# Performance work log

Measured on AMD Instinct MI355X. Metric: run time of the kernel, lower is better.

## Reference

```python
import jax, jax.numpy as jnp
import numpy as np

B, T, V, S = 64, 512, 1296, 32
BLANK = 0
NEG = jnp.float32(-1e30)  # log-space -inf surrogate (keeps grads finite)


def setup_inputs() -> dict:
    key = jax.random.key(0)
    k1, k2 = jax.random.split(key)
    logits = jax.random.normal(k1, (B, T, V), dtype=jnp.float32)
    # CTC targets must not contain the blank index (0)
    targets = jax.random.randint(k2, (B, S), 1, V).astype(jnp.int64)
    input_lengths = jnp.full((B,), T, dtype=jnp.int32)
    target_lengths = jnp.full((B,), S, dtype=jnp.int32)
    return {"logits": logits, "targets": targets,
            "input_lengths": input_lengths, "target_lengths": target_lengths}


def _ctc_loss(log_probs, targets, input_lengths, target_lengths):
    """CTC negative log-likelihood, reduction='mean' (per-sample / target_len, then batch mean)."""
    Bb, Tt, Vv = log_probs.shape
    Ss = targets.shape[1]
    L = 2 * Ss + 1  # extended label sequence: blank-interleaved

    ext = jnp.full((Bb, L), BLANK, dtype=targets.dtype).at[:, 1::2].set(targets)  # (B,L)
    # log-prob of each extended label at each time: (B,T,L)
    lp_ext = jnp.take_along_axis(log_probs, jnp.broadcast_to(ext[:, None, :], (Bb, Tt, L)), axis=2)

    # transition s-2 -> s allowed iff ext[s] is non-blank (s odd) and ext[s] != ext[s-2]
    pos = jnp.arange(L)
    ext_m2 = jnp.pad(ext, ((0, 0), (2, 0)), constant_values=-1)[:, :L]
    skip_ok = (pos[None, :] % 2 == 1) & (ext != ext_m2)  # (B,L)

    alpha0 = (jnp.full((Bb, L), NEG)
              .at[:, 0].set(lp_ext[:, 0, 0])
              .at[:, 1].set(lp_ext[:, 0, 1]))

    def step(alpha, lp_t):
        a1 = alpha
        a2 = jnp.pad(alpha[:, :-1], ((0, 0), (1, 0)), constant_values=NEG)
        a3 = jnp.where(skip_ok, jnp.pad(alpha[:, :-2], ((0, 0), (2, 0)), constant_values=NEG), NEG)
        new = jnp.logaddexp(jnp.logaddexp(a1, a2), a3) + lp_t
        return new, new

    _, alphas_rest = jax.lax.scan(step, alpha0, jnp.swapaxes(lp_ext, 0, 1)[1:])  # (T-1,B,L)
    alphas = jnp.concatenate([alpha0[None], alphas_rest], axis=0)  # (T,B,L)

    bi = jnp.arange(Bb)
    alpha_last = alphas[input_lengths - 1, bi]  # (B,L)
    l_end = alpha_last[bi, 2 * target_lengths]       # final blank
    l_lab = alpha_last[bi, 2 * target_lengths - 1]   # final label
    nll = -jnp.logaddexp(l_end, l_lab)               # (B,)
    nll = jnp.where(jnp.isinf(nll) | (nll > 1e29), 0.0, nll)  # zero_infinity=True
    return jnp.mean(nll / target_lengths.astype(nll.dtype))    # reduction='mean'


def reference(logits, targets, input_lengths, target_lengths):
    log_probs = jax.nn.log_softmax(logits, axis=-1)
    return _ctc_loss(log_probs, targets, input_lengths, target_lengths)
```

## Files before the change

kernel.cpp:

```cpp
#include <hip/hip_runtime.h>
#include <math.h>

#define BB 64
#define TT 512
#define VV 1296
#define SS 32
#define NST 64
#define NG  (TT/4)
#define NEGV (-1e30f)
#define LOG2E 1.44269504088896340736f
#define LN2   0.69314718055994530942f

#define EXP2(x) __builtin_amdgcn_exp2f(x)
#define LOG2(x) __builtin_amdgcn_logf(x)

__device__ __forceinline__ float dpp_shr1(float old, float src) {
    return __int_as_float(__builtin_amdgcn_update_dpp(
        __float_as_int(old), __float_as_int(src), 0x138, 0xf, 0xf, false));
}
__device__ __forceinline__ float dpp_shl1(float old, float src) {
    return __int_as_float(__builtin_amdgcn_update_dpp(
        __float_as_int(old), __float_as_int(src), 0x130, 0xf, 0xf, false));
}

template<int CTRL>
__device__ __forceinline__ float dpp_add(float s) {
    return s + __int_as_float(__builtin_amdgcn_update_dpp(
        0, __float_as_int(s), CTRL, 0xf, 0xf, false));
}
__device__ __forceinline__ float wave_sum63(float s) {
    s = dpp_add<0x111>(s);
    s = dpp_add<0x112>(s);
    s = dpp_add<0x114>(s);
    s = dpp_add<0x118>(s);
    s = dpp_add<0x142>(s);
    s = dpp_add<0x143>(s);
    return s;
}

__device__ __forceinline__ float expsum_row(
    float4 a0, float4 a1, float4 a2, float4 a3, float4 a4, float4 ax, int lane)
{
    if (lane >= 4) { ax.x = NEGV; ax.y = NEGV; ax.z = NEGV; ax.w = NEGV; }
    const float t0 = (__expf(a0.x) + __expf(a0.y)) + (__expf(a0.z) + __expf(a0.w));
    const float t1 = (__expf(a1.x) + __expf(a1.y)) + (__expf(a1.z) + __expf(a1.w));
    const float t2 = (__expf(a2.x) + __expf(a2.y)) + (__expf(a2.z) + __expf(a2.w));
    const float t3 = (__expf(a3.x) + __expf(a3.y)) + (__expf(a3.z) + __expf(a3.w));
    const float t4 = (__expf(a4.x) + __expf(a4.y)) + (__expf(a4.z) + __expf(a4.w));
    const float t5 = (__expf(ax.x) + __expf(ax.y)) + (__expf(ax.z) + __expf(ax.w));
    return ((t0 + t1) + (t2 + t3)) + (t4 + t5);
}

__device__ __forceinline__ float finish_row(float s, float g) {
    const float tot = __shfl(wave_sum63(s), 63, 64);
    return __builtin_fmaf(g, LOG2E, -LOG2(tot));
}

__global__ __launch_bounds__(256, 4) void k_lse_gather(
    const float* __restrict__ logits,
    const int* __restrict__ targets,
    float* __restrict__ lp_ext,
    float* __restrict__ out)
{
    const int wid  = threadIdx.x >> 6;
    const int lane = threadIdx.x & 63;
    const int W    = blockIdx.x * 4 + wid;
    const int b    = W >> 7;
    const int g    = W & (NG - 1);

    if (W == 0 && lane == 0) out[0] = 0.f;

    const int lab = (lane & 1) ? 0 : targets[b * SS + (lane >> 1)];

    const float* rowbase = logits + (size_t)(b * TT + g * 4) * VV;
    const float4* r0 = (const float4*)(rowbase);
    const float4* r1 = (const float4*)(rowbase + VV);
    const float4* r2 = (const float4*)(rowbase + 2 * VV);
    const float4* r3 = (const float4*)(rowbase + 3 * VV);

    float4 A0 = r0[lane], A1 = r0[lane + 64], A2 = r0[lane + 128],
           A3 = r0[lane + 192], A4 = r0[lane + 256], Ax = r0[320 + (lane & 3)];
    float  Ag = ((const float*)r0)[lab];
    float4 B0 = r1[lane], B1 = r1[lane + 64], B2 = r1[lane + 128],
           B3 = r1[lane + 192], B4 = r1[lane + 256], Bx = r1[320 + (lane & 3)];
    float  Bg = ((const float*)r1)[lab];
    float4 C0 = r2[lane], C1 = r2[lane + 64], C2 = r2[lane + 128],
           C3 = r2[lane + 192], C4 = r2[lane + 256], Cx = r2[320 + (lane & 3)];
    float  Cg = ((const float*)r2)[lab];
    float4 D0 = r3[lane], D1 = r3[lane + 64], D2 = r3[lane + 128],
           D3 = r3[lane + 192], D4 = r3[lane + 256], Dx = r3[320 + (lane & 3)];
    float  Dg = ((const float*)r3)[lab];

    __builtin_amdgcn_sched_barrier(0);

    const float sA = expsum_row(A0, A1, A2, A3, A4, Ax, lane);
    const float lp0 = finish_row(sA, Ag);
    const float sB = expsum_row(B0, B1, B2, B3, B4, Bx, lane);
    const float lp1 = finish_row(sB, Bg);
    const float sC = expsum_row(C0, C1, C2, C3, C4, Cx, lane);
    const float lp2 = finish_row(sC, Cg);
    const float sD = expsum_row(D0, D1, D2, D3, D4, Dx, lane);
    const float lp3 = finish_row(sD, Dg);

    float4 st; st.x = lp0; st.y = lp1; st.z = lp2; st.w = lp3;
    ((float4*)lp_ext)[(size_t)W * NST + lane] = st;
}

#define PFV 6

__global__ __launch_bounds__(64) void k_alpha(
    const float* __restrict__ lp_ext,
    const int* __restrict__ targets,
    const int* __restrict__ in_len,
    const int* __restrict__ tgt_len,
    float* __restrict__ out)
{
    const int b    = blockIdx.x;
    const int lane = threadIdx.x;
    const float4* lpv = (const float4*)(lp_ext + (size_t)b * NG * NST * 4);
    const int Ti = in_len[b];
    const int Sb = tgt_len[b];

    bool skip = false;
    if (!(lane & 1) && lane >= 2) {
        const int j = lane >> 1;
        skip = (targets[b * SS + j] != targets[b * SS + j - 1]);
    }

    const float4 g0 = lpv[lane];

    float alpha = (lane == 0) ? g0.x : NEGV;
    float c0    = __shfl(g0.x, 1, 64);

#define STEP(LPS)                                                            \
    {                                                                        \
        const float lps_ = (LPS);                                            \
           \
        const float lpbk_ = (lane & 1) ? lps_ : dpp_shl1(lps_, lps_);        \
        const float a1_ = alpha;                                             \
        const float a2_ = dpp_shr1(c0, alpha);         \
        float a3_       = dpp_shr1(NEGV, a2_);               \
        a3_ = skip ? a3_ : NEGV;          \
        c0 += lpbk_;                                     \
        const float mx_ = fmaxf(fmaxf(a1_, a2_), a3_);           \
        const float ml_ = mx_ + lps_;                 \
        alpha = LOG2(EXP2(a1_ - mx_) + EXP2(a2_ - mx_) +                     \
                     EXP2(a3_ - mx_)) + ml_;                                 \
    }

    if (Ti > 1) STEP(g0.y);
    if (Ti > 2) STEP(g0.z);
    if (Ti > 3) STEP(g0.w);

    float4 bufv[PFV];
    #pragma unroll
    for (int i = 0; i < PFV; ++i) {
        int gg = 1 + i; if (gg > NG - 1) gg = NG - 1;
        bufv[i] = lpv[gg * NST + lane];
    }

    int g = 1;
    while (g + PFV <= NG) {
        #pragma unroll
        for (int i = 0; i < PFV; ++i) {
            const float4 cur = bufv[i];
            int gp = g + i + PFV; if (gp > NG - 1) gp = NG - 1;
            bufv[i] = lpv[(size_t)gp * NST + lane];
            const int t0 = (g + i) * 4;
            if (t0 + 3 < Ti) {
                STEP(cur.x); STEP(cur.y); STEP(cur.z); STEP(cur.w);
            } else {
                if (t0 + 0 < Ti) STEP(cur.x);
                if (t0 + 1 < Ti) STEP(cur.y);
                if (t0 + 2 < Ti) STEP(cur.z);
                if (t0 + 3 < Ti) STEP(cur.w);
            }
        }
        g += PFV;
    }
    #pragma unroll
    for (int i = 0; i < PFV; ++i) {
        const int gi = g + i;
        if (gi <= NG - 1) {
            const float4 cur = bufv[i];
            const int t0 = gi * 4;
            if (t0 + 3 < Ti) {
                STEP(cur.x); STEP(cur.y); STEP(cur.z); STEP(cur.w);
            } else {
                if (t0 + 0 < Ti) STEP(cur.x);
                if (t0 + 1 < Ti) STEP(cur.y);
                if (t0 + 2 < Ti) STEP(cur.z);
                if (t0 + 3 < Ti) STEP(cur.w);
            }
        }
    }
#undef STEP

    const float vll = __shfl(alpha, 2 * Sb - 2, 64);
    const float vle = __shfl(alpha, 2 * Sb - 1, 64);

    if (lane == 0) {
        const float mx = fmaxf(vle, vll);
        float nll = -LN2 * (mx + LOG2(EXP2(vle - mx) + EXP2(vll - mx)));
        if (isinf(nll) || nll > 1e29f) nll = 0.f;
        atomicAdd(out, nll / ((float)Sb * (float)BB));
    }
}

extern "C" void kernel_launch(void* const* d_in, const int* in_sizes, int n_in,
                              void* d_out, int out_size, void* d_ws, size_t ws_size,
                              hipStream_t stream) {
    const float* logits   = (const float*)d_in[0];
    const int*   targets  = (const int*)d_in[1];
    const int*   in_len   = (const int*)d_in[2];
    const int*   tgt_len  = (const int*)d_in[3];
    float*       out      = (float*)d_out;

    float* lp_ext = (float*)d_ws;

    k_lse_gather<<<BB * NG / 4, 256, 0, stream>>>(logits, targets, lp_ext, out);
    k_alpha<<<BB, 64, 0, stream>>>(lp_ext, targets, in_len, tgt_len, out);
}
```

Measured before the change: 272.7 us.

## Process eight rows per wave in LSE kernel with rotating 3-row load pipeline

Each wave now handles 8 time rows instead of 4. Loads are software-pipelined across three rotating register buffers, so the loads for the next rows are issued while earlier rows are being reduced. The goal is to hide memory latency inside a wave rather than relying on occupancy, and the grid is halved to match. The trade-off is fewer waves in flight and higher register pressure.

```diff
diff --git a/kernel.cpp b/kernel.cpp
--- a/kernel.cpp
+++ b/kernel.cpp
@@ -64,46 +64,58 @@
 {
     const int wid  = threadIdx.x >> 6;
     const int lane = threadIdx.x & 63;
-    const int W    = blockIdx.x * 4 + wid;
-    const int b    = W >> 7;
-    const int g    = W & (NG - 1);
-
-    if (W == 0 && lane == 0) out[0] = 0.f;
+    const int Wp   = blockIdx.x * 4 + wid;
+    const int b    = Wp >> 6;
+    const int u    = Wp & 63;
+    const int t0   = u * 8;
+
+    if (Wp == 0 && lane == 0) out[0] = 0.f;
 
     const int lab = (lane & 1) ? 0 : targets[b * SS + (lane >> 1)];
 
-    const float* rowbase = logits + (size_t)(b * TT + g * 4) * VV;
-    const float4* r0 = (const float4*)(rowbase);
-    const float4* r1 = (const float4*)(rowbase + VV);
-    const float4* r2 = (const float4*)(rowbase + 2 * VV);
-    const float4* r3 = (const float4*)(rowbase + 3 * VV);
-
-    float4 A0 = r0[lane], A1 = r0[lane + 64], A2 = r0[lane + 128],
-           A3 = r0[lane + 192], A4 = r0[lane + 256], Ax = r0[320 + (lane & 3)];
-    float  Ag = ((const float*)r0)[lab];
-    float4 B0 = r1[lane], B1 = r1[lane + 64], B2 = r1[lane + 128],
-           B3 = r1[lane + 192], B4 = r1[lane + 256], Bx = r1[320 + (lane & 3)];
-    float  Bg = ((const float*)r1)[lab];
-    float4 C0 = r2[lane], C1 = r2[lane + 64], C2 = r2[lane + 128],
-           C3 = r2[lane + 192], C4 = r2[lane + 256], Cx = r2[320 + (lane & 3)];
-    float  Cg = ((const float*)r2)[lab];
-    float4 D0 = r3[lane], D1 = r3[lane + 64], D2 = r3[lane + 128],
-           D3 = r3[lane + 192], D4 = r3[lane + 256], Dx = r3[320 + (lane & 3)];
-    float  Dg = ((const float*)r3)[lab];
-
-    __builtin_amdgcn_sched_barrier(0);
-
-    const float sA = expsum_row(A0, A1, A2, A3, A4, Ax, lane);
-    const float lp0 = finish_row(sA, Ag);
-    const float sB = expsum_row(B0, B1, B2, B3, B4, Bx, lane);
-    const float lp1 = finish_row(sB, Bg);
-    const float sC = expsum_row(C0, C1, C2, C3, C4, Cx, lane);
-    const float lp2 = finish_row(sC, Cg);
-    const float sD = expsum_row(D0, D1, D2, D3, D4, Dx, lane);
-    const float lp3 = finish_row(sD, Dg);
-
-    float4 st; st.x = lp0; st.y = lp1; st.z = lp2; st.w = lp3;
-    ((float4*)lp_ext)[(size_t)W * NST + lane] = st;
+    const float* rb = logits + ((size_t)(b * TT + t0)) * VV;
+
+#define LOADROW(P, T)                                                        \
+    {                                                                        \
+        const float4* r4_ = (const float4*)(rb + (size_t)(T) * VV);          \
+        (P##0) = r4_[lane];        (P##1) = r4_[lane + 64];                  \
+        (P##2) = r4_[lane + 128];  (P##3) = r4_[lane + 192];                 \
+        (P##4) = r4_[lane + 256];  (P##x) = r4_[320 + (lane & 3)];           \
+        (P##g) = ((const float*)r4_)[lab];                                   \
+    }
+#define CONSUME(P) finish_row(expsum_row((P##0), (P##1), (P##2), (P##3),     \
+                                         (P##4), (P##x), lane), (P##g))
+#define SB __builtin_amdgcn_sched_barrier(0);
+
+    float4 A0, A1, A2, A3, A4, Ax;  float Ag;
+    float4 B0, B1, B2, B3, B4, Bx;  float Bg;
+    float4 C0, C1, C2, C3, C4, Cx;  float Cg;
+
+    LOADROW(A, 0) LOADROW(B, 1) LOADROW(C, 2) SB
+
+    const float lp0 = CONSUME(A);  LOADROW(A, 3) SB
+    const float lp1 = CONSUME(B);  LOADROW(B, 4) SB
+    const float lp2 = CONSUME(C);  LOADROW(C, 5) SB
+    const float lp3 = CONSUME(A);  LOADROW(A, 6) SB
+
+    {
+        float4 st; st.x = lp0; st.y = lp1; st.z = lp2; st.w = lp3;
+        ((float4*)lp_ext)[((size_t)(b * NG) + (t0 >> 2)) * NST + lane] = st;
+    }
+
+    const float lp4 = CONSUME(B);  LOADROW(B, 7) SB
+    const float lp5 = CONSUME(C);
+    const float lp6 = CONSUME(A);
+    const float lp7 = CONSUME(B);
+
+    {
+        float4 st; st.x = lp4; st.y = lp5; st.z = lp6; st.w = lp7;
+        ((float4*)lp_ext)[((size_t)(b * NG) + (t0 >> 2) + 1) * NST + lane] = st;
+    }
+
+#undef LOADROW
+#undef CONSUME
+#undef SB
 }
 
 #define PFV 6
@@ -218,6 +230,6 @@
 
     float* lp_ext = (float*)d_ws;
 
-    k_lse_gather<<<BB * NG / 4, 256, 0, stream>>>(logits, targets, lp_ext, out);
+    k_lse_gather<<<BB * NG / 8, 256, 0, stream>>>(logits, targets, lp_ext, out);
     k_alpha<<<BB, 64, 0, stream>>>(lp_ext, targets, in_len, tgt_len, out);
 }
```

New measurement: 273.3 us. Within noise of the previous version (+0.2%).
